# Performance work log

Hardware: AMD Instinct MI355X
Metric: run time of the kernel (lower is better)

## Reference

```python
import jax, jax.numpy as jnp
import numpy as np

B, T_TXT, T_IMG, N_LAT = 4, 2048, 8, 64
DIM, DIM_VIS, HEADS, DIM_HEAD = 2048, 1024, 8, 64
INNER = HEADS * DIM_HEAD
LN_EPS = 1e-5


def setup_inputs() -> dict:
    key = jax.random.key(0)
    ks = jax.random.split(key, 8)
    x = jax.random.normal(ks[0], (B, T_TXT, DIM), dtype=jnp.float32)
    media = jax.random.normal(ks[1], (B, T_IMG, N_LAT, DIM_VIS), dtype=jnp.float32)
    # exactly T_IMG media tokens per batch row at random positions
    pos = jax.random.randint(ks[2], (B, T_IMG), 0, T_TXT)
    media_locations = jnp.zeros((B, T_TXT), dtype=bool).at[jnp.arange(B)[:, None], pos].set(True)
    gamma = jnp.ones((DIM,), dtype=jnp.float32)
    beta = jnp.zeros((DIM,), dtype=jnp.float32)
    Wq = jax.random.normal(ks[3], (DIM, INNER), dtype=jnp.float32) * 0.02
    Wkv = jax.random.normal(ks[4], (DIM_VIS, 2 * INNER), dtype=jnp.float32) * 0.02
    Wout = jax.random.normal(ks[5], (INNER, DIM), dtype=jnp.float32) * 0.02
    return {"x": x, "media": media, "media_locations": media_locations,
            "gamma": gamma, "beta": beta, "Wq": Wq, "Wkv": Wkv, "Wout": Wout}


def _split_heads(t, h):
    b, s, _ = t.shape
    return t.reshape(b, s, h, -1).transpose(0, 2, 1, 3)  # b h s d


def reference(x, media, media_locations, gamma, beta, Wq, Wkv, Wout):
    b, t_txt, _ = x.shape
    _, t_img, n, _ = media.shape
    scale = DIM_HEAD ** (-0.5)

    # LayerNorm
    mu = jnp.mean(x, axis=-1, keepdims=True)
    var = jnp.mean(jnp.square(x - mu), axis=-1, keepdims=True)
    xn = (x - mu) * jax.lax.rsqrt(var + LN_EPS) * gamma + beta

    q = _split_heads(xn @ Wq, HEADS) * scale                # b h i d
    media_f = media.reshape(b, t_img * n, -1)               # b (t n) dv
    kv = media_f @ Wkv
    k, v = jnp.split(kv, 2, axis=-1)
    k = _split_heads(k, HEADS)                              # b h j d
    v = _split_heads(v, HEADS)

    sim = jnp.einsum('bhid,bhjd->bhij', q, k)               # b h i (t n)

    text_time = jnp.cumsum(media_locations.astype(jnp.int32), axis=-1)   # b i
    media_time = jnp.repeat(jnp.arange(1, t_img + 1), n)                 # (t n)
    mask = text_time[:, None, :, None] == media_time[None, None, None, :]

    neg = -jnp.finfo(sim.dtype).max
    sim = jnp.where(mask, sim, neg)
    sim = sim - jax.lax.stop_gradient(jnp.max(sim, axis=-1, keepdims=True))
    attn = jax.nn.softmax(sim, axis=-1)
    # zero attention for text tokens that precede any media
    attn = jnp.where((text_time == 0)[:, None, :, None], 0.0, attn)

    out = jnp.einsum('bhij,bhjd->bhid', attn, v)
    out = out.transpose(0, 2, 1, 3).reshape(b, t_txt, INNER)
    return out @ Wout
```

## Files before the change

kernel.cpp:

```cpp
#include <hip/hip_runtime.h>
#include <hip/hip_bf16.h>
#include <stdint.h>

typedef __bf16 bf16_t;
typedef __bf16 bf16x8 __attribute__((ext_vector_type(8)));
typedef float f32x4 __attribute__((ext_vector_type(4)));

#define NB      4
#define T_TXT   2048
#define T_IMG   8
#define N_LAT   64
#define DIM     2048
#define DIM_VIS 1024
#define HEADS   8
#define DHEAD   64
#define INNER   512

__device__ __forceinline__ void gld_lds16(const void* g, void* l) {
    __builtin_amdgcn_global_load_lds((const __attribute__((address_space(1))) void*)g,
                                     (__attribute__((address_space(3))) void*)l,
                                     16, 0, 0);
}

__global__ __launch_bounds__(256) void transpose3_k(const float* __restrict__ Wq,
                                                    const float* __restrict__ Wkv,
                                                    const float* __restrict__ Wout,
                                                    bf16_t* __restrict__ WqT,
                                                    bf16_t* __restrict__ WkvT,
                                                    bf16_t* __restrict__ WoutT) {
    __shared__ float tile[32][33];
    const float* in; bf16_t* out; int R, C;
    int which = blockIdx.y;
    if (which == 0)      { in = Wq;   out = WqT;   R = 2048; C = 512;  }
    else if (which == 1) { in = Wkv;  out = WkvT;  R = 1024; C = 1024; }
    else                 { in = Wout; out = WoutT; R = 512;  C = 2048; }
    int nbx = C >> 5;
    int bx = blockIdx.x % nbx, by = blockIdx.x / nbx;
    int c0 = bx * 32, r0 = by * 32;
    int x = threadIdx.x, y = threadIdx.y;
#pragma unroll
    for (int d = 0; d < 4; d++)
        tile[y + d * 8][x] = in[(size_t)(r0 + y + d * 8) * C + c0 + x];
    __syncthreads();
#pragma unroll
    for (int d = 0; d < 4; d++)
        out[(size_t)(c0 + y + d * 8) * R + r0 + x] = (bf16_t)tile[x][y + d * 8];
}

__global__ __launch_bounds__(256) void cvt_k(const float* __restrict__ in,
                                             bf16_t* __restrict__ out) {
    int idx = (blockIdx.x * 256 + threadIdx.x) * 8;
    f32x4 a = *(const f32x4*)(in + idx);
    f32x4 b = *(const f32x4*)(in + idx + 4);
    bf16x8 o;
#pragma unroll
    for (int i = 0; i < 4; i++) { o[i] = (bf16_t)a[i]; o[i + 4] = (bf16_t)b[i]; }
    *(bf16x8*)(out + idx) = o;
}

__global__ __launch_bounds__(256) void ln_k(const float* __restrict__ x,
                                            const float* __restrict__ gamma,
                                            const float* __restrict__ beta,
                                            bf16_t* __restrict__ xn) {
    int row = blockIdx.x;
    int t = threadIdx.x;
    const float* xp = x + (size_t)row * DIM + t * 8;
    f32x4 v0 = *(const f32x4*)xp;
    f32x4 v1 = *(const f32x4*)(xp + 4);
    float f[8];
    float s = 0.f, ss = 0.f;
#pragma unroll
    for (int i = 0; i < 4; i++) { f[i] = v0[i]; f[i + 4] = v1[i]; }
#pragma unroll
    for (int i = 0; i < 8; i++) { s += f[i]; ss += f[i] * f[i]; }
#pragma unroll
    for (int off = 32; off > 0; off >>= 1) { s += __shfl_xor(s, off); ss += __shfl_xor(ss, off); }
    __shared__ float sbuf[4], sbuf2[4];
    int wid = t >> 6, lane = t & 63;
    if (lane == 0) { sbuf[wid] = s; sbuf2[wid] = ss; }
    __syncthreads();
    s  = sbuf[0] + sbuf[1] + sbuf[2] + sbuf[3];
    ss = sbuf2[0] + sbuf2[1] + sbuf2[2] + sbuf2[3];
    float mu  = s * (1.0f / DIM);
    float var = ss * (1.0f / DIM) - mu * mu;
    float rs  = rsqrtf(var + 1e-5f);
    f32x4 g0 = *(const f32x4*)(gamma + t * 8);
    f32x4 g1 = *(const f32x4*)(gamma + t * 8 + 4);
    f32x4 b0 = *(const f32x4*)(beta + t * 8);
    f32x4 b1 = *(const f32x4*)(beta + t * 8 + 4);
    bf16x8 o;
#pragma unroll
    for (int i = 0; i < 4; i++) {
        o[i]     = (bf16_t)((f[i]     - mu) * rs * g0[i] + b0[i]);
        o[i + 4] = (bf16_t)((f[i + 4] - mu) * rs * g1[i] + b1[i]);
    }
    *(bf16x8*)(xn + (size_t)row * DIM + t * 8) = o;
}

template <typename OT>
__device__ __forceinline__ void gemm_body(const bf16_t* __restrict__ A,
                                          const bf16_t* __restrict__ Bt,
                                          OT* __restrict__ C,
                                          int M, int N, int K, int Kper,
                                          float scale, int bid,
                                          int gx, int gy, int gz,
                                          bf16_t* lA, bf16_t* lB) {
    int tid = threadIdx.x;
    int w = tid >> 6, lane = tid & 63;
    int wm = w >> 1, wn = w & 1;

    int nwg = gx * gy * gz;
    int cpx = nwg >> 3;
    int nid = (bid & 7) * cpx + (bid >> 3);
    int tpy = gx * gz;
    int by = nid / tpy;
    int rr = nid - by * tpy;
    int bz = rr / gx;
    int bx = rr - bz * gx;

    int bm0 = by * 128, bn0 = bx * 128;
    int kbase = bz * Kper;
    int q = lane >> 4, l16 = lane & 15;

    int l15 = lane & 15, lq = lane >> 4;
    const bf16_t* pA0 = A  + (size_t)(bm0 + w * 16      + l15) * K + kbase + lq * 8;
    const bf16_t* pA1 = A  + (size_t)(bm0 + 64 + w * 16 + l15) * K + kbase + lq * 8;
    const bf16_t* pB0 = Bt + (size_t)(bn0 + w * 16      + l15) * K + kbase + lq * 8;
    const bf16_t* pB1 = Bt + (size_t)(bn0 + 64 + w * 16 + l15) * K + kbase + lq * 8;

    f32x4 acc[4][4];
#pragma unroll
    for (int i = 0; i < 4; i++)
#pragma unroll
        for (int j = 0; j < 4; j++)
            acc[i][j] = (f32x4){0.f, 0.f, 0.f, 0.f};

    auto stage = [&](int buf, int k0) {
        gld_lds16(pA0 + k0, lA + buf * 4096 + w * 512);
        gld_lds16(pA1 + k0, lA + buf * 4096 + 2048 + w * 512);
        gld_lds16(pB0 + k0, lB + buf * 4096 + w * 512);
        gld_lds16(pB1 + k0, lB + buf * 4096 + 2048 + w * 512);
    };
    auto compute = [&](int buf) {
        bf16x8 af[4], bfr[4];
#pragma unroll
        for (int mt = 0; mt < 4; mt++)
            af[mt] = *(const bf16x8*)(lA + buf * 4096 + (wm * 4 + mt) * 512 + q * 128 + l16 * 8);
#pragma unroll
        for (int nt = 0; nt < 4; nt++)
            bfr[nt] = *(const bf16x8*)(lB + buf * 4096 + (wn * 4 + nt) * 512 + q * 128 + l16 * 8);
#pragma unroll
        for (int mt = 0; mt < 4; mt++)
#pragma unroll
            for (int nt = 0; nt < 4; nt++)
                acc[mt][nt] = __builtin_amdgcn_mfma_f32_16x16x32_bf16(af[mt], bfr[nt], acc[mt][nt], 0, 0, 0);
    };

    stage(0, 0);
    __syncthreads();
    int cur = 0;
    for (int k0 = 32; k0 < Kper; k0 += 32) {
        stage(cur ^ 1, k0);
        compute(cur);
        __syncthreads();
        cur ^= 1;
    }
    compute(cur);

    OT* Cz = C + (size_t)bz * M * N;
#pragma unroll
    for (int mt = 0; mt < 4; mt++)
#pragma unroll
        for (int nt = 0; nt < 4; nt++)
#pragma unroll
            for (int r = 0; r < 4; r++) {
                int row = bm0 + wm * 64 + mt * 16 + q * 4 + r;
                int col = bn0 + wn * 64 + nt * 16 + l16;
                Cz[(size_t)row * N + col] = (OT)(acc[mt][nt][r] * scale);
            }
}

__global__ __launch_bounds__(256) void gemm12_k(const bf16_t* __restrict__ xn,
                                                const bf16_t* __restrict__ WqT,
                                                bf16_t* __restrict__ part,
                                                const bf16_t* __restrict__ mediab,
                                                const bf16_t* __restrict__ WkvT,
                                                bf16_t* __restrict__ kvbuf) {
    __shared__ __align__(16) bf16_t lA[2 * 4096];
    __shared__ __align__(16) bf16_t lB[2 * 4096];
    int bid = blockIdx.x;
    if (bid < 1024)
        gemm_body<bf16_t>(xn, WqT, part, 8192, 512, 2048, 512, 1.0f, bid, 4, 64, 4, lA, lB);
    else
        gemm_body<bf16_t>(mediab, WkvT, kvbuf, 2048, 1024, 1024, 1024, 1.0f, bid - 1024, 8, 16, 1, lA, lB);
}

__global__ __launch_bounds__(256) void gemm3_k(const bf16_t* __restrict__ aout,
                                               const bf16_t* __restrict__ WoutT,
                                               float* __restrict__ out) {
    __shared__ __align__(16) bf16_t lA[2 * 4096];
    __shared__ __align__(16) bf16_t lB[2 * 4096];
    gemm_body<float>(aout, WoutT, out, 8192, 2048, 512, 512, 1.0f, blockIdx.x, 16, 64, 1, lA, lB);
}

__global__ __launch_bounds__(256) void reduce4_k(const bf16_t* __restrict__ p,
                                                 bf16_t* __restrict__ o,
                                                 size_t n, float scale) {
    size_t i = ((size_t)blockIdx.x * 256 + threadIdx.x) * 8;
    bf16x8 a0 = *(const bf16x8*)(p + i);
    bf16x8 a1 = *(const bf16x8*)(p + n + i);
    bf16x8 a2 = *(const bf16x8*)(p + 2 * n + i);
    bf16x8 a3 = *(const bf16x8*)(p + 3 * n + i);
    bf16x8 r;
#pragma unroll
    for (int u = 0; u < 8; u++)
        r[u] = (bf16_t)(((float)a0[u] + (float)a1[u] + (float)a2[u] + (float)a3[u]) * scale);
    *(bf16x8*)(o + i) = r;
}

__global__ __launch_bounds__(256) void cumsum_bucket_k(const void* __restrict__ locs,
                                                       int* __restrict__ bstart,
                                                       int* __restrict__ bcnt) {
    int b = blockIdx.x, t = threadIdx.x;
    const unsigned* up = (const unsigned*)locs;
    const int* ip = (const int*)locs;
    const unsigned char* bp = (const unsigned char*)locs;
    const float* fp = (const float*)locs;

    int other = 0, nf = 0;
#pragma unroll
    for (int i = 0; i < 8; i++) {
        unsigned wv = up[t * 8 + i];
        nf    += (wv == 0x3F800000u);
        other += (wv != 0u && wv != 1u && wv != 0x3F800000u);
    }
#pragma unroll
    for (int off = 32; off > 0; off >>= 1) { other += __shfl_xor(other, off); nf += __shfl_xor(nf, off); }
    __shared__ int so[4], sf[4];
    int wid = t >> 6, lane = t & 63;
    if (lane == 0) { so[wid] = other; sf[wid] = nf; }
    __syncthreads();
    other = so[0] + so[1] + so[2] + so[3];
    nf    = sf[0] + sf[1] + sf[2] + sf[3];
    int mode = (other > 0) ? 0 : ((nf > 0) ? 2 : 1);

    int v[8];
    int s = 0;
#pragma unroll
    for (int i = 0; i < 8; i++) {
        int idx = b * T_TXT + t * 8 + i;
        int xv;
        if (mode == 1)      xv = ip[idx];
        else if (mode == 0) xv = (int)bp[idx];
        else                xv = (fp[idx] != 0.f) ? 1 : 0;
        v[i] = xv;
        s += xv;
    }
    __shared__ int sc[256];
    __shared__ int sstart[T_IMG];
    if (t < T_IMG) sstart[t] = T_TXT;
    sc[t] = s;
    __syncthreads();
    for (int off = 1; off < 256; off <<= 1) {
        int add = (t >= off) ? sc[t - off] : 0;
        __syncthreads();
        sc[t] += add;
        __syncthreads();
    }
    int run = sc[t] - s;
#pragma unroll
    for (int i = 0; i < 8; i++) {
        run += v[i];
        if (v[i] && run <= T_IMG) sstart[run - 1] = t * 8 + i;
    }
    __syncthreads();
    if (t < T_IMG) {
        int st = sstart[t];
        int nx = (t + 1 < T_IMG) ? sstart[t + 1] : T_TXT;
        bstart[b * T_IMG + t] = st;
        bcnt[b * T_IMG + t]   = nx - st;
    }
}

__global__ __launch_bounds__(256) void attn_mfma_k(const bf16_t* __restrict__ q,
                                                   const bf16_t* __restrict__ kv,
                                                   const int* __restrict__ bstart,
                                                   const int* __restrict__ bcnt,
                                                   bf16_t* __restrict__ aout) {
    __shared__ __align__(16) bf16_t lK[64 * 64];
    __shared__ __align__(16) bf16_t lVt[64 * 64];
    __shared__ __align__(16) bf16_t lP[4][16 * 64];

    int bid = blockIdx.x;
    int bucket = bid >> 6;
    int h = (bid >> 3) & 7;
    int c = bid & 7;
    int n_q = bcnt[bucket];
    int qlo = c << 8;
    if (n_q <= qlo) return;
    int qhi = (n_q < qlo + 256) ? n_q : (qlo + 256);
    int b = bucket >> 3;
    int timg = bucket & 7;
    int row0 = b * T_TXT + bstart[bucket];
    size_t krow0 = (size_t)(b * (T_IMG * N_LAT) + timg * N_LAT);

    int tid = threadIdx.x;
    int wid = tid >> 6, lane = tid & 63;
    int quad = lane >> 4, l16 = lane & 15;

    {
        const bf16_t* s0 = kv + (krow0 + 16 * wid + (lane >> 3)) * (2 * INNER) + h * DHEAD + (lane & 7) * 8;
        const bf16_t* s1 = kv + (krow0 + 16 * wid + 8 + (lane >> 3)) * (2 * INNER) + h * DHEAD + (lane & 7) * 8;
        gld_lds16(s0, lK + wid * 1024);
        gld_lds16(s1, lK + wid * 1024 + 512);
    }
    {
        int key = tid & 63, dblk = tid >> 6;
        const bf16_t* vsrc = kv + (krow0 + key) * (2 * INNER) + INNER + h * DHEAD + dblk * 16;
        bf16x8 v0 = *(const bf16x8*)vsrc;
        bf16x8 v1 = *(const bf16x8*)(vsrc + 8);
#pragma unroll
        for (int u = 0; u < 8; u++) {
            lVt[(dblk * 16 + u) * 64 + key]     = v0[u];
            lVt[(dblk * 16 + 8 + u) * 64 + key] = v1[u];
        }
    }
    __syncthreads();

    for (int c0 = qlo + wid * 16; c0 < qhi; c0 += 64) {
        int qi = row0 + c0 + ((c0 + l16 < n_q) ? l16 : 0);

        const bf16_t* qrow = q + (size_t)qi * INNER + h * DHEAD + quad * 8;
        bf16x8 qf0 = *(const bf16x8*)qrow;
        bf16x8 qf1 = *(const bf16x8*)(qrow + 32);
        f32x4 s[4];
#pragma unroll
        for (int nt = 0; nt < 4; nt++) s[nt] = (f32x4){0.f, 0.f, 0.f, 0.f};
#pragma unroll
        for (int nt = 0; nt < 4; nt++) {
            bf16x8 kf0 = *(const bf16x8*)(lK + (l16 + 16 * nt) * 64 + quad * 8);
            bf16x8 kf1 = *(const bf16x8*)(lK + (l16 + 16 * nt) * 64 + 32 + quad * 8);
            s[nt] = __builtin_amdgcn_mfma_f32_16x16x32_bf16(qf0, kf0, s[nt], 0, 0, 0);
            s[nt] = __builtin_amdgcn_mfma_f32_16x16x32_bf16(qf1, kf1, s[nt], 0, 0, 0);
        }

        float mr[4];
#pragma unroll
        for (int r = 0; r < 4; r++) {
            float m = fmaxf(fmaxf(s[0][r], s[1][r]), fmaxf(s[2][r], s[3][r]));
#pragma unroll
            for (int off = 8; off >= 1; off >>= 1) m = fmaxf(m, __shfl_xor(m, off));
            mr[r] = m;
        }
        float p[4][4];
#pragma unroll
        for (int nt = 0; nt < 4; nt++)
#pragma unroll
            for (int r = 0; r < 4; r++)
                p[nt][r] = __expf(s[nt][r] - mr[r]);
#pragma unroll
        for (int r = 0; r < 4; r++) {
            float tsum = p[0][r] + p[1][r] + p[2][r] + p[3][r];
#pragma unroll
            for (int off = 8; off >= 1; off >>= 1) tsum += __shfl_xor(tsum, off);
            float inv = 1.0f / tsum;
            p[0][r] *= inv; p[1][r] *= inv; p[2][r] *= inv; p[3][r] *= inv;
        }

        bf16_t* pt = lP[wid];
#pragma unroll
        for (int nt = 0; nt < 4; nt++)
#pragma unroll
            for (int r = 0; r < 4; r++)
                pt[(quad * 4 + r) * 64 + 16 * nt + l16] = (bf16_t)p[nt][r];
        asm volatile("s_waitcnt lgkmcnt(0)" ::: "memory");

        bf16x8 pf0 = *(const bf16x8*)(pt + l16 * 64 + quad * 8);
        bf16x8 pf1 = *(const bf16x8*)(pt + l16 * 64 + 32 + quad * 8);
        f32x4 o[4];
#pragma unroll
        for (int ntd = 0; ntd < 4; ntd++) o[ntd] = (f32x4){0.f, 0.f, 0.f, 0.f};
#pragma unroll
        for (int ntd = 0; ntd < 4; ntd++) {
            bf16x8 vf0 = *(const bf16x8*)(lVt + (l16 + 16 * ntd) * 64 + quad * 8);
            bf16x8 vf1 = *(const bf16x8*)(lVt + (l16 + 16 * ntd) * 64 + 32 + quad * 8);
            o[ntd] = __builtin_amdgcn_mfma_f32_16x16x32_bf16(pf0, vf0, o[ntd], 0, 0, 0);
            o[ntd] = __builtin_amdgcn_mfma_f32_16x16x32_bf16(pf1, vf1, o[ntd], 0, 0, 0);
        }

#pragma unroll
        for (int r = 0; r < 4; r++) {
            int qidx = c0 + quad * 4 + r;
            if (qidx < n_q) {
                bf16_t* op = aout + (size_t)(row0 + qidx) * INNER + h * DHEAD + l16;
#pragma unroll
                for (int ntd = 0; ntd < 4; ntd++)
                    op[16 * ntd] = (bf16_t)o[ntd][r];
            }
        }
    }
}

extern "C" void kernel_launch(void* const* d_in, const int* in_sizes, int n_in,
                              void* d_out, int out_size, void* d_ws, size_t ws_size,
                              hipStream_t stream) {
    const float* x     = (const float*)d_in[0];
    const float* media = (const float*)d_in[1];
    const void*  locs  = d_in[2];
    const float* gamma = (const float*)d_in[3];
    const float* beta  = (const float*)d_in[4];
    const float* Wq    = (const float*)d_in[5];
    const float* Wkv   = (const float*)d_in[6];
    const float* Wout  = (const float*)d_in[7];
    float* out = (float*)d_out;

    bf16_t* xn   = (bf16_t*)d_out;
    bf16_t* part = (bf16_t*)d_out + (size_t)16 * 1024 * 1024;

    char* p = (char*)d_ws;
    bf16_t* qbuf   = (bf16_t*)p; p += (size_t)8192 * 512 * 2;
    bf16_t* aout   = (bf16_t*)p; p += (size_t)8192 * 512 * 2;
    bf16_t* kvbuf  = (bf16_t*)p; p += (size_t)2048 * 1024 * 2;
    bf16_t* mediab = (bf16_t*)p; p += (size_t)2048 * 1024 * 2;
    bf16_t* WqT    = (bf16_t*)p; p += (size_t)512 * 2048 * 2;
    bf16_t* WkvT   = (bf16_t*)p; p += (size_t)1024 * 1024 * 2;
    bf16_t* WoutT  = (bf16_t*)p; p += (size_t)2048 * 512 * 2;
    int*    bstart = (int*)p;    p += 32 * sizeof(int);
    int*    bcnt   = (int*)p;    p += 32 * sizeof(int);

    transpose3_k<<<dim3(1024, 3), dim3(32, 8), 0, stream>>>(Wq, Wkv, Wout, WqT, WkvT, WoutT);
    cvt_k<<<(2048 * 1024) / (256 * 8), 256, 0, stream>>>(media, mediab);

    ln_k<<<8192, 256, 0, stream>>>(x, gamma, beta, xn);

    gemm12_k<<<1152, 256, 0, stream>>>(xn, WqT, part, mediab, WkvT, kvbuf);
    reduce4_k<<<2048, 256, 0, stream>>>(part, qbuf, (size_t)8192 * 512, 0.125f);

    cumsum_bucket_k<<<NB, 256, 0, stream>>>(locs, bstart, bcnt);

    hipMemsetAsync(aout, 0, (size_t)8192 * 512 * 2, stream);

    attn_mfma_k<<<32 * HEADS * 8, 256, 0, stream>>>(qbuf, kvbuf, bstart, bcnt, aout);

    gemm3_k<<<1024, 256, 0, stream>>>(aout, WoutT, out);
}
```

Before: 283.2 us.

## Enlarge GEMM tiles to 256x256 with 512-thread blocks and split-K the KV projection

The shared GEMM body now computes 256x256 output tiles with 8 waves per block, each wave holding an 8x4 grid of MFMA accumulators, so each staged LDS tile is reused more and global loads per FLOP drop. The KV projection is switched to a 4-way split-K. Its partial results are written into the Q buffer as scratch and then summed by an extra reduce pass. The cumsum kernel is moved to the start of the launch sequence. In exchange the blocks use more registers and LDS, and the output GEMM launches far fewer blocks, which risks occupancy and wave-quantization losses.

Measured after the change: 265.0 us. 1.07x faster.

```diff
diff --git a/kernel.cpp b/kernel.cpp
--- a/kernel.cpp
+++ b/kernel.cpp
@@ -98,16 +98,16 @@
 }
 
 template <typename OT>
-__device__ __forceinline__ void gemm_body(const bf16_t* __restrict__ A,
-                                          const bf16_t* __restrict__ Bt,
-                                          OT* __restrict__ C,
-                                          int M, int N, int K, int Kper,
-                                          float scale, int bid,
-                                          int gx, int gy, int gz,
-                                          bf16_t* lA, bf16_t* lB) {
+__device__ __forceinline__ void gemm_body256(const bf16_t* __restrict__ A,
+                                             const bf16_t* __restrict__ Bt,
+                                             OT* __restrict__ C,
+                                             int M, int N, int K, int Kper,
+                                             float scale, int bid,
+                                             int gx, int gy, int gz,
+                                             bf16_t* lA, bf16_t* lB) {
     int tid = threadIdx.x;
     int w = tid >> 6, lane = tid & 63;
-    int wm = w >> 1, wn = w & 1;
+    int wm = w >> 2, wn = w & 3;
 
     int nwg = gx * gy * gz;
     int cpx = nwg >> 3;
@@ -118,39 +118,38 @@
     int bz = rr / gx;
     int bx = rr - bz * gx;
 
-    int bm0 = by * 128, bn0 = bx * 128;
+    int bm0 = by * 256, bn0 = bx * 256;
     int kbase = bz * Kper;
     int q = lane >> 4, l16 = lane & 15;
 
-    int l15 = lane & 15, lq = lane >> 4;
-    const bf16_t* pA0 = A  + (size_t)(bm0 + w * 16      + l15) * K + kbase + lq * 8;
-    const bf16_t* pA1 = A  + (size_t)(bm0 + 64 + w * 16 + l15) * K + kbase + lq * 8;
-    const bf16_t* pB0 = Bt + (size_t)(bn0 + w * 16      + l15) * K + kbase + lq * 8;
-    const bf16_t* pB1 = Bt + (size_t)(bn0 + 64 + w * 16 + l15) * K + kbase + lq * 8;
-
-    f32x4 acc[4][4];
-#pragma unroll
-    for (int i = 0; i < 4; i++)
+    const bf16_t* pA0 = A  + (size_t)(bm0 + w * 32      + l16) * K + kbase + q * 8;
+    const bf16_t* pA1 = A  + (size_t)(bm0 + w * 32 + 16 + l16) * K + kbase + q * 8;
+    const bf16_t* pB0 = Bt + (size_t)(bn0 + w * 32      + l16) * K + kbase + q * 8;
+    const bf16_t* pB1 = Bt + (size_t)(bn0 + w * 32 + 16 + l16) * K + kbase + q * 8;
+
+    f32x4 acc[8][4];
+#pragma unroll
+    for (int i = 0; i < 8; i++)
 #pragma unroll
         for (int j = 0; j < 4; j++)
             acc[i][j] = (f32x4){0.f, 0.f, 0.f, 0.f};
 
     auto stage = [&](int buf, int k0) {
-        gld_lds16(pA0 + k0, lA + buf * 4096 + w * 512);
-        gld_lds16(pA1 + k0, lA + buf * 4096 + 2048 + w * 512);
-        gld_lds16(pB0 + k0, lB + buf * 4096 + w * 512);
-        gld_lds16(pB1 + k0, lB + buf * 4096 + 2048 + w * 512);
+        gld_lds16(pA0 + k0, lA + buf * 8192 + (w * 2)     * 512);
+        gld_lds16(pA1 + k0, lA + buf * 8192 + (w * 2 + 1) * 512);
+        gld_lds16(pB0 + k0, lB + buf * 8192 + (w * 2)     * 512);
+        gld_lds16(pB1 + k0, lB + buf * 8192 + (w * 2 + 1) * 512);
     };
     auto compute = [&](int buf) {
-        bf16x8 af[4], bfr[4];
-#pragma unroll
-        for (int mt = 0; mt < 4; mt++)
-            af[mt] = *(const bf16x8*)(lA + buf * 4096 + (wm * 4 + mt) * 512 + q * 128 + l16 * 8);
+        bf16x8 af[8], bfr[4];
+#pragma unroll
+        for (int mt = 0; mt < 8; mt++)
+            af[mt] = *(const bf16x8*)(lA + buf * 8192 + (wm * 8 + mt) * 512 + q * 128 + l16 * 8);
 #pragma unroll
         for (int nt = 0; nt < 4; nt++)
-            bfr[nt] = *(const bf16x8*)(lB + buf * 4096 + (wn * 4 + nt) * 512 + q * 128 + l16 * 8);
-#pragma unroll
-        for (int mt = 0; mt < 4; mt++)
+            bfr[nt] = *(const bf16x8*)(lB + buf * 8192 + (wn * 4 + nt) * 512 + q * 128 + l16 * 8);
+#pragma unroll
+        for (int mt = 0; mt < 8; mt++)
 #pragma unroll
             for (int nt = 0; nt < 4; nt++)
                 acc[mt][nt] = __builtin_amdgcn_mfma_f32_16x16x32_bf16(af[mt], bfr[nt], acc[mt][nt], 0, 0, 0);
@@ -169,38 +168,38 @@
 
     OT* Cz = C + (size_t)bz * M * N;
 #pragma unroll
-    for (int mt = 0; mt < 4; mt++)
+    for (int mt = 0; mt < 8; mt++)
 #pragma unroll
         for (int nt = 0; nt < 4; nt++)
 #pragma unroll
             for (int r = 0; r < 4; r++) {
-                int row = bm0 + wm * 64 + mt * 16 + q * 4 + r;
+                int row = bm0 + wm * 128 + mt * 16 + q * 4 + r;
                 int col = bn0 + wn * 64 + nt * 16 + l16;
                 Cz[(size_t)row * N + col] = (OT)(acc[mt][nt][r] * scale);
             }
 }
 
-__global__ __launch_bounds__(256) void gemm12_k(const bf16_t* __restrict__ xn,
-                                                const bf16_t* __restrict__ WqT,
-                                                bf16_t* __restrict__ part,
-                                                const bf16_t* __restrict__ mediab,
-                                                const bf16_t* __restrict__ WkvT,
-                                                bf16_t* __restrict__ kvbuf) {
-    __shared__ __align__(16) bf16_t lA[2 * 4096];
-    __shared__ __align__(16) bf16_t lB[2 * 4096];
+__global__ __launch_bounds__(512, 2) void gemm12_k(const bf16_t* __restrict__ xn,
+                                                   const bf16_t* __restrict__ WqT,
+                                                   bf16_t* __restrict__ part,
+                                                   const bf16_t* __restrict__ mediab,
+                                                   const bf16_t* __restrict__ WkvT,
+                                                   bf16_t* __restrict__ kvpart) {
+    __shared__ __align__(16) bf16_t lA[2 * 8192];
+    __shared__ __align__(16) bf16_t lB[2 * 8192];
     int bid = blockIdx.x;
-    if (bid < 1024)
-        gemm_body<bf16_t>(xn, WqT, part, 8192, 512, 2048, 512, 1.0f, bid, 4, 64, 4, lA, lB);
+    if (bid < 128)
+        gemm_body256<bf16_t>(mediab, WkvT, kvpart, 2048, 1024, 1024, 256, 1.0f, bid, 4, 8, 4, lA, lB);
     else
-        gemm_body<bf16_t>(mediab, WkvT, kvbuf, 2048, 1024, 1024, 1024, 1.0f, bid - 1024, 8, 16, 1, lA, lB);
-}
-
-__global__ __launch_bounds__(256) void gemm3_k(const bf16_t* __restrict__ aout,
-                                               const bf16_t* __restrict__ WoutT,
-                                               float* __restrict__ out) {
-    __shared__ __align__(16) bf16_t lA[2 * 4096];
-    __shared__ __align__(16) bf16_t lB[2 * 4096];
-    gemm_body<float>(aout, WoutT, out, 8192, 2048, 512, 512, 1.0f, blockIdx.x, 16, 64, 1, lA, lB);
+        gemm_body256<bf16_t>(xn, WqT, part, 8192, 512, 2048, 512, 1.0f, bid - 128, 2, 32, 4, lA, lB);
+}
+
+__global__ __launch_bounds__(512, 2) void gemm3_k(const bf16_t* __restrict__ aout,
+                                                  const bf16_t* __restrict__ WoutT,
+                                                  float* __restrict__ out) {
+    __shared__ __align__(16) bf16_t lA[2 * 8192];
+    __shared__ __align__(16) bf16_t lB[2 * 8192];
+    gemm_body256<float>(aout, WoutT, out, 8192, 2048, 512, 512, 1.0f, blockIdx.x, 8, 32, 1, lA, lB);
 }
 
 __global__ __launch_bounds__(256) void reduce4_k(const bf16_t* __restrict__ p,
@@ -428,19 +427,20 @@
     int*    bstart = (int*)p;    p += 32 * sizeof(int);
     int*    bcnt   = (int*)p;    p += 32 * sizeof(int);
 
+    cumsum_bucket_k<<<NB, 256, 0, stream>>>(locs, bstart, bcnt);
     transpose3_k<<<dim3(1024, 3), dim3(32, 8), 0, stream>>>(Wq, Wkv, Wout, WqT, WkvT, WoutT);
     cvt_k<<<(2048 * 1024) / (256 * 8), 256, 0, stream>>>(media, mediab);
 
     ln_k<<<8192, 256, 0, stream>>>(x, gamma, beta, xn);
 
-    gemm12_k<<<1152, 256, 0, stream>>>(xn, WqT, part, mediab, WkvT, kvbuf);
+    gemm12_k<<<384, 512, 0, stream>>>(xn, WqT, part, mediab, WkvT, qbuf);
+
+    reduce4_k<<<1024, 256, 0, stream>>>(qbuf, kvbuf, (size_t)2048 * 1024, 1.0f);
     reduce4_k<<<2048, 256, 0, stream>>>(part, qbuf, (size_t)8192 * 512, 0.125f);
 
-    cumsum_bucket_k<<<NB, 256, 0, stream>>>(locs, bstart, bcnt);
-
     hipMemsetAsync(aout, 0, (size_t)8192 * 512 * 2, stream);
 
     attn_mfma_k<<<32 * HEADS * 8, 256, 0, stream>>>(qbuf, kvbuf, bstart, bcnt, aout);
 
-    gemm3_k<<<1024, 256, 0, stream>>>(aout, WoutT, out);
-}
+    gemm3_k<<<256, 512, 0, stream>>>(aout, WoutT, out);
+}
```
